# Performance work log

Hardware: AMD Instinct MI355X
Metric: run time of the kernel (lower is better)

## Reference

```python
import jax, jax.numpy as jnp
import numpy as np

N = 50000
E = 800000
IN_CH = 128
HIDDEN = 32
HEADS = 4
OUT_CH = 64
NEG_SLOPE = 0.2


def setup_inputs() -> dict:
    key = jax.random.key(0)
    ks = jax.random.split(key, 12)
    x = jax.random.normal(ks[0], (N, IN_CH), dtype=jnp.float32)
    edge_index = jax.random.randint(ks[1], (2, E), 0, N, dtype=jnp.int64)
    # layer 1: GATConv(IN_CH, HIDDEN, heads=4, concat=True)
    s1 = 1.0 / np.sqrt(IN_CH)
    W1 = jax.random.normal(ks[2], (IN_CH, HEADS * HIDDEN), dtype=jnp.float32) * s1
    att_src1 = jax.random.normal(ks[3], (HEADS, HIDDEN), dtype=jnp.float32) * 0.1
    att_dst1 = jax.random.normal(ks[4], (HEADS, HIDDEN), dtype=jnp.float32) * 0.1
    b1 = jnp.zeros((HEADS * HIDDEN,), dtype=jnp.float32)
    # layer 2: GATConv(HEADS*HIDDEN, OUT_CH, heads=1, concat=False)
    s2 = 1.0 / np.sqrt(HEADS * HIDDEN)
    W2 = jax.random.normal(ks[5], (HEADS * HIDDEN, OUT_CH), dtype=jnp.float32) * s2
    att_src2 = jax.random.normal(ks[6], (1, OUT_CH), dtype=jnp.float32) * 0.1
    att_dst2 = jax.random.normal(ks[7], (1, OUT_CH), dtype=jnp.float32) * 0.1
    b2 = jnp.zeros((OUT_CH,), dtype=jnp.float32)
    return {"x": x, "edge_index": edge_index, "W1": W1, "att_src1": att_src1,
            "att_dst1": att_dst1, "b1": b1, "W2": W2, "att_src2": att_src2,
            "att_dst2": att_dst2, "b2": b2}


def gat_conv(x, src, dst, W, a_src, a_dst, bias, heads, out_ch, concat):
    n = x.shape[0]
    h = (x @ W).reshape(n, heads, out_ch)               # [N, H, C]
    alpha_s = jnp.sum(h * a_src[None], axis=-1)          # [N, H]
    alpha_d = jnp.sum(h * a_dst[None], axis=-1)          # [N, H]
    e = alpha_s[src] + alpha_d[dst]                      # [E, H]
    e = jnp.where(e > 0, e, NEG_SLOPE * e)               # leaky_relu(0.2)
    # segment softmax over incoming edges of each dst node
    e_max = jax.ops.segment_max(e, dst, num_segments=n)
    e_max = jnp.where(jnp.isfinite(e_max), e_max, 0.0)
    ex = jnp.exp(e - e_max[dst])
    denom = jax.ops.segment_sum(ex, dst, num_segments=n)
    alpha = ex / (denom[dst] + 1e-16)                    # [E, H]
    msg = h[src] * alpha[:, :, None]                     # [E, H, C]
    out = jax.ops.segment_sum(msg, dst, num_segments=n)  # [N, H, C]
    if concat:
        out = out.reshape(n, heads * out_ch)
    else:
        out = out.mean(axis=1)
    return out + bias


def reference(x, edge_index, W1, att_src1, att_dst1, b1, W2, att_src2, att_dst2, b2):
    n = x.shape[0]
    loop = jnp.arange(n, dtype=edge_index.dtype)
    src = jnp.concatenate([edge_index[0], loop])  # add self-loops (PyG default)
    dst = jnp.concatenate([edge_index[1], loop])
    h = gat_conv(x, src, dst, W1, att_src1, att_dst1, b1, HEADS, HIDDEN, True)
    h = jax.nn.elu(h)
    return gat_conv(h, src, dst, W2, att_src2, att_dst2, b2, 1, OUT_CH, False)
```

## Files before the change

kernel.cpp:

```cpp
#include <hip/hip_runtime.h>

#define NN    50000
#define NE    800000
#define NET   850000
#define NBUCK ((NN + 255) / 256)
#define MAXB  8192
#define BINB  256
#define AGGB  3125

typedef __fp16 half2_t __attribute__((ext_vector_type(2)));
typedef _Float16 half8 __attribute__((ext_vector_type(8)));
typedef float floatx4 __attribute__((ext_vector_type(4)));

__device__ __forceinline__ float lrelu(float v) { return fmaxf(v, 0.2f * v); }
__device__ __forceinline__ unsigned pk16(float a, float b) {
    half2_t h = __builtin_amdgcn_cvt_pkrtz(a, b);
    return __builtin_bit_cast(unsigned, h);
}
__device__ __forceinline__ float2 unpk16(unsigned u) {
    half2_t h = __builtin_bit_cast(half2_t, u);
    return make_float2((float)h.x, (float)h.y);
}

__global__ __launch_bounds__(256) void gemm1_mfma_kernel(
    const float* __restrict__ x, const _Float16* __restrict__ w1t,
    const float* __restrict__ att_s, const float* __restrict__ att_d,
    _Float16* __restrict__ h1h, float* __restrict__ as, float* __restrict__ ad)
{
    __shared__ _Float16 lw[128 * 128];
    __shared__ _Float16 hs[64 * 128];
    const int t    = threadIdx.x;
    const int lane = t & 63;
    const int m    = lane & 15;
    const int q    = lane >> 4;
    const int wv   = t >> 6;
    const int gr0  = blockIdx.x * 64;
    const int rbase = gr0 + wv * 16;

    const int rme = rbase + m;
    const int rc  = rme < NN ? rme : NN - 1;
    const float* ap = x + (size_t)rc * 128 + q * 8;

    float4 f0[4], f1[4];
#pragma unroll
    for (int ks = 0; ks < 4; ks++) {
        f0[ks] = *(const float4*)(ap + ks * 32);
        f1[ks] = *(const float4*)(ap + ks * 32 + 4);
    }

    {
        const int kb = t & 15;
        const int n0 = t >> 4;
#pragma unroll
        for (int it = 0; it < 8; it++) {
            const int n = n0 + it * 16;
            const uint4 v = *(const uint4*)(w1t + n * 128 + kb * 8);
            *(uint4*)((char*)lw + n * 256 + ((kb * 16) ^ ((n & 7) << 4))) = v;
        }
    }
    __syncthreads();

    floatx4 acc[8];
#pragma unroll
    for (int nt = 0; nt < 8; nt++) acc[nt] = (floatx4){0.f, 0.f, 0.f, 0.f};

    const int swz = (m & 7) << 4;
#pragma unroll
    for (int ks = 0; ks < 4; ks++) {
        const uint4 au = make_uint4(pk16(f0[ks].x, f0[ks].y), pk16(f0[ks].z, f0[ks].w),
                                    pk16(f1[ks].x, f1[ks].y), pk16(f1[ks].z, f1[ks].w));
        const half8 a = __builtin_bit_cast(half8, au);
#pragma unroll
        for (int nt = 0; nt < 8; nt++) {
            const int n = nt * 16 + m;
            const half8 b = *(const half8*)((const char*)lw + n * 256 +
                                            ((ks * 64 + q * 16) ^ swz));
            acc[nt] = __builtin_amdgcn_mfma_f32_16x16x32_f16(a, b, acc[nt], 0, 0, 0);
        }
    }

    const int lrow0 = wv * 16 + q * 4;
#pragma unroll
    for (int nt = 0; nt < 8; nt++)
#pragma unroll
        for (int r = 0; r < 4; r++)
            hs[(lrow0 + r) * 128 + nt * 16 + m] = (_Float16)acc[nt][r];
    __syncthreads();

#pragma unroll
    for (int i = t; i < 1024; i += 256) {
        const int row = i >> 4;
        if (gr0 + row < NN)
            ((half8*)h1h)[(size_t)(gr0 + row) * 16 + (i & 15)] = ((const half8*)hs)[i];
    }

    const int arow = t >> 2, hd = t & 3;
    const int grow = gr0 + arow;
    float ps = 0.f, pd = 0.f;
    const half8*  hp8 = (const half8*)(hs + arow * 128 + hd * 32);
    const float4* s4  = (const float4*)(att_s + hd * 32);
    const float4* d4  = (const float4*)(att_d + hd * 32);
#pragma unroll
    for (int cc = 0; cc < 4; cc++) {
        const half8 hv = hp8[cc];
        const float4 a = s4[cc * 2], b = s4[cc * 2 + 1];
        const float4 c = d4[cc * 2], e = d4[cc * 2 + 1];
        ps += (float)hv[0]*a.x + (float)hv[1]*a.y + (float)hv[2]*a.z + (float)hv[3]*a.w
            + (float)hv[4]*b.x + (float)hv[5]*b.y + (float)hv[6]*b.z + (float)hv[7]*b.w;
        pd += (float)hv[0]*c.x + (float)hv[1]*c.y + (float)hv[2]*c.z + (float)hv[3]*c.w
            + (float)hv[4]*e.x + (float)hv[5]*e.y + (float)hv[6]*e.z + (float)hv[7]*e.w;
    }
    if (grow < NN) {
        as[grow * 4 + hd] = ps;
        ad[grow * 4 + hd] = pd;
    }
}

__global__ __launch_bounds__(256) void gemm2_mfma_kernel(
    const _Float16* __restrict__ ah, const _Float16* __restrict__ w2t,
    const float* __restrict__ att_s, const float* __restrict__ att_d,
    _Float16* __restrict__ h2h, float* __restrict__ as, float* __restrict__ ad)
{
    __shared__ _Float16 lw[64 * 128];
    __shared__ _Float16 hs[64 * 64];
    const int t    = threadIdx.x;
    const int lane = t & 63;
    const int m    = lane & 15;
    const int q    = lane >> 4;
    const int wv   = t >> 6;
    const int gr0  = blockIdx.x * 64;
    const int rbase = gr0 + wv * 16;

    const int rme = rbase + m;
    const int rc  = rme < NN ? rme : NN - 1;
    const _Float16* ap = ah + (size_t)rc * 128 + q * 8;

    half8 av[4];
#pragma unroll
    for (int ks = 0; ks < 4; ks++) av[ks] = *(const half8*)(ap + ks * 32);

    {
        const int kb = t & 15;
        const int n0 = t >> 4;
#pragma unroll
        for (int it = 0; it < 4; it++) {
            const int n = n0 + it * 16;
            const uint4 v = *(const uint4*)(w2t + n * 128 + kb * 8);
            *(uint4*)((char*)lw + n * 256 + ((kb * 16) ^ ((n & 7) << 4))) = v;
        }
    }
    __syncthreads();

    floatx4 acc[4];
#pragma unroll
    for (int nt = 0; nt < 4; nt++) acc[nt] = (floatx4){0.f, 0.f, 0.f, 0.f};

    const int swz = (m & 7) << 4;
#pragma unroll
    for (int ks = 0; ks < 4; ks++) {
#pragma unroll
        for (int nt = 0; nt < 4; nt++) {
            const int n = nt * 16 + m;
            const half8 b = *(const half8*)((const char*)lw + n * 256 +
                                            ((ks * 64 + q * 16) ^ swz));
            acc[nt] = __builtin_amdgcn_mfma_f32_16x16x32_f16(av[ks], b, acc[nt], 0, 0, 0);
        }
    }

    const int lrow0 = wv * 16 + q * 4;
#pragma unroll
    for (int nt = 0; nt < 4; nt++)
#pragma unroll
        for (int r = 0; r < 4; r++)
            hs[(lrow0 + r) * 64 + nt * 16 + m] = (_Float16)acc[nt][r];
    __syncthreads();

#pragma unroll
    for (int i = t; i < 512; i += 256) {
        const int row = i >> 3;
        if (gr0 + row < NN)
            ((half8*)h2h)[(size_t)(gr0 + row) * 8 + (i & 7)] = ((const half8*)hs)[i];
    }

    const int arow = t >> 2, sg = t & 3;
    const int grow = gr0 + arow;
    float ps = 0.f, pd = 0.f;
    const half8*  hp8 = (const half8*)(hs + arow * 64 + sg * 16);
    const float4* s4  = (const float4*)(att_s + sg * 16);
    const float4* d4  = (const float4*)(att_d + sg * 16);
#pragma unroll
    for (int cc = 0; cc < 2; cc++) {
        const half8 hv = hp8[cc];
        const float4 a = s4[cc * 2], b = s4[cc * 2 + 1];
        const float4 c = d4[cc * 2], e = d4[cc * 2 + 1];
        ps += (float)hv[0]*a.x + (float)hv[1]*a.y + (float)hv[2]*a.z + (float)hv[3]*a.w
            + (float)hv[4]*b.x + (float)hv[5]*b.y + (float)hv[6]*b.z + (float)hv[7]*b.w;
        pd += (float)hv[0]*c.x + (float)hv[1]*c.y + (float)hv[2]*c.z + (float)hv[3]*c.w
            + (float)hv[4]*e.x + (float)hv[5]*e.y + (float)hv[6]*e.z + (float)hv[7]*e.w;
    }
    ps += __shfl_down(ps, 2);  pd += __shfl_down(pd, 2);
    ps += __shfl_down(ps, 1);  pd += __shfl_down(pd, 1);
    if (sg == 0 && grow < NN) { as[grow] = ps; ad[grow] = pd; }
}

__global__ __launch_bounds__(1024) void bin_kernel(const int* __restrict__ ei,
                                                   const float* __restrict__ W1,
                                                   const float* __restrict__ W2,
                                                   _Float16* __restrict__ w1t,
                                                   _Float16* __restrict__ w2t,
                                                   int* __restrict__ bcnt,
                                                   unsigned* __restrict__ pairs)
{
    if (blockIdx.x < 24) {
        const int idx = blockIdx.x * 1024 + threadIdx.x;
        if (idx < 16384) {
            const int k = idx >> 7, n = idx & 127;
            w1t[n * 128 + k] = (_Float16)W1[idx];
        } else {
            const int j = idx - 16384;
            const int k = j >> 6, n = j & 63;
            w2t[n * 128 + k] = (_Float16)W2[j];
        }
    }

    __shared__ int hist[NBUCK], base[NBUCK], cur[NBUCK];
    const int t = threadIdx.x;
    if (t < NBUCK) { hist[t] = 0; cur[t] = 0; }
    __syncthreads();

    for (int e = blockIdx.x * 1024 + t; e < NET; e += BINB * 1024) {
        const int d = (e < NE) ? ei[NE + e] : (e - NE);
        atomicAdd(&hist[d >> 8], 1);
    }
    __syncthreads();
    if (t < NBUCK && hist[t]) base[t] = atomicAdd(&bcnt[t * 16], hist[t]);
    __syncthreads();
    for (int e = blockIdx.x * 1024 + t; e < NET; e += BINB * 1024) {
        int s, d;
        if (e < NE) { s = ei[e]; d = ei[NE + e]; } else { s = d = e - NE; }
        const int bk = d >> 8;
        const int r = atomicAdd(&cur[bk], 1);
        pairs[(size_t)bk * MAXB + base[bk] + r] =
            (unsigned)s | ((unsigned)(d & 255) << 16);
    }
}

__global__ __launch_bounds__(1024) void bsort_kernel(
    const int* __restrict__ bcnt, const unsigned* __restrict__ pairs,
    int* __restrict__ row_beg, int* __restrict__ row_end,
    int* __restrict__ col)
{
    __shared__ int hist[256], cur[256], sh[256];
    __shared__ int outl[MAXB];
    const int b = blockIdx.x, t = threadIdx.x;
    const int m = bcnt[b * 16];
    const int gbase = b * MAXB;
    if (t < 256) hist[t] = 0;
    __syncthreads();
    for (int i = t; i < m; i += 1024)
        atomicAdd(&hist[pairs[gbase + i] >> 16], 1);
    __syncthreads();
    if (t < 256) sh[t] = hist[t];
    __syncthreads();
#pragma unroll
    for (int off = 1; off < 256; off <<= 1) {
        int u = (t < 256 && t >= off) ? sh[t - off] : 0;
        __syncthreads();
        if (t < 256) sh[t] += u;
        __syncthreads();
    }
    if (t < 256) {
        const int ex = sh[t] - hist[t];
        cur[t] = ex;
        const int node = (b << 8) + t;
        if (node < NN) {
            row_beg[node] = gbase + ex;
            row_end[node] = gbase + ex + hist[t];
        }
    }
    __syncthreads();
    for (int i = t; i < m; i += 1024) {
        const unsigned p = pairs[gbase + i];
        const int r = atomicAdd(&cur[p >> 16], 1);
        outl[r] = (int)(p & 0xFFFFu);
    }
    __syncthreads();
    for (int i = t; i < m; i += 1024) col[gbase + i] = outl[i];
}

__global__ __launch_bounds__(1024) void agg1_fused_kernel(
    const int* __restrict__ row_beg, const int* __restrict__ row_end,
    const int* __restrict__ col, const unsigned* __restrict__ hh,
    const float* __restrict__ as1, const float* __restrict__ ad1,
    const float* __restrict__ b1, unsigned* __restrict__ acth)
{
    __shared__ float wbuf[16][64 * 4];
    const int wv   = threadIdx.x >> 6;
    const int d    = __builtin_amdgcn_readfirstlane(blockIdx.x * 16 + wv);
    const int lane = threadIdx.x & 63;
    const int head = lane >> 4;
    const int beg = row_beg[d], end = row_end[d];
    const float4 ad4 = ((const float4*)ad1)[d];
    float* wb = wbuf[wv];

    float acc0 = 0.f, acc1 = 0.f, den = 0.f;

    for (int jb = beg; jb < end; jb += 64) {
        const int cnt = min(64, end - jb);
        {
            const int sl = col[jb + min(lane, cnt - 1)];
            const float4 a = ((const float4*)as1)[sl];
            float4 w4;
            w4.x = __expf(lrelu(a.x + ad4.x));
            w4.y = __expf(lrelu(a.y + ad4.y));
            w4.z = __expf(lrelu(a.z + ad4.z));
            w4.w = __expf(lrelu(a.w + ad4.w));
            ((float4*)wb)[lane] = w4;
        }
        __asm__ volatile("s_waitcnt lgkmcnt(0)" ::: "memory");

        int k = 0;
        for (; k + 16 <= cnt; k += 16) {
            float    w[16];
            unsigned g[16];
#pragma unroll
            for (int u = 0; u < 16; u++) {
                const int s = col[jb + k + u];
                w[u] = wb[(k + u) * 4 + head];
                g[u] = hh[s * 64 + lane];
            }
#pragma unroll
            for (int u = 0; u < 16; u++) {
                const float2 g2 = unpk16(g[u]);
                den  += w[u];
                acc0 += w[u] * g2.x;
                acc1 += w[u] * g2.y;
            }
        }
        for (; k + 4 <= cnt; k += 4) {
            float    w[4];
            unsigned g[4];
#pragma unroll
            for (int u = 0; u < 4; u++) {
                const int s = col[jb + k + u];
                w[u] = wb[(k + u) * 4 + head];
                g[u] = hh[s * 64 + lane];
            }
#pragma unroll
            for (int u = 0; u < 4; u++) {
                const float2 g2 = unpk16(g[u]);
                den  += w[u];
                acc0 += w[u] * g2.x;
                acc1 += w[u] * g2.y;
            }
        }
        for (; k < cnt; k++) {
            const float w = wb[k * 4 + head];
            const float2 g2 = unpk16(hh[col[jb + k] * 64 + lane]);
            den  += w;
            acc0 += w * g2.x;
            acc1 += w * g2.y;
        }
        __asm__ volatile("" ::: "memory");
    }
    const float2 bb  = ((const float2*)b1)[lane];
    const float  inv = 1.f / (den + 1e-16f);
    float v0 = acc0 * inv + bb.x;
    float v1 = acc1 * inv + bb.y;
    v0 = v0 > 0.f ? v0 : (__expf(v0) - 1.f);
    v1 = v1 > 0.f ? v1 : (__expf(v1) - 1.f);
    acth[d * 64 + lane] = pk16(v0, v1);
}

__global__ __launch_bounds__(1024) void agg2_fused_kernel(
    const int* __restrict__ row_beg, const int* __restrict__ row_end,
    const int* __restrict__ col, const _Float16* __restrict__ h,
    const float* __restrict__ as2, const float* __restrict__ ad2,
    const float* __restrict__ b2, float* __restrict__ out)
{
    __shared__ float wbuf[16][64];
    const int wv   = threadIdx.x >> 6;
    const int d    = __builtin_amdgcn_readfirstlane(blockIdx.x * 16 + wv);
    const int lane = threadIdx.x & 63;
    const int half = lane >> 5;
    const int c    = lane & 31;
    const int beg = row_beg[d], end = row_end[d];
    const float add = ad2[d];
    float* wb = wbuf[wv];
    const unsigned* __restrict__ h2 = (const unsigned*)h;

    float acc0 = 0.f, acc1 = 0.f, den = 0.f;

    for (int jb = beg; jb < end; jb += 64) {
        const int cnt = min(64, end - jb);
        {
            const int sl = col[jb + min(lane, cnt - 1)];
            wb[lane] = __expf(lrelu(as2[sl] + add));
        }
        __asm__ volatile("s_waitcnt lgkmcnt(0)" ::: "memory");

        int k = 0;
        for (; k + 16 <= cnt; k += 16) {
            float    w[8];
            unsigned g[8];
#pragma unroll
            for (int u = 0; u < 8; u++) {
                const int e = jb + k + 2 * u + half;
                const int s = col[e];
                w[u] = wb[k + 2 * u + half];
                g[u] = h2[(size_t)s * 32 + c];
            }
#pragma unroll
            for (int u = 0; u < 8; u++) {
                const float2 g2 = unpk16(g[u]);
                den  += w[u];
                acc0 += w[u] * g2.x;
                acc1 += w[u] * g2.y;
            }
        }
        for (; k < cnt; k += 2) {
            const int  e   = k + half;
            const bool ok  = e < cnt;
            const int  s   = col[jb + (ok ? e : cnt - 1)];
            const float w  = ok ? wb[e] : 0.f;
            const float2 g2 = unpk16(h2[(size_t)s * 32 + c]);
            den  += w;
            acc0 += w * g2.x;
            acc1 += w * g2.y;
        }
        __asm__ volatile("" ::: "memory");
    }
    acc0 += __shfl_xor(acc0, 32);
    acc1 += __shfl_xor(acc1, 32);
    den  += __shfl_xor(den, 32);

    if (half == 0) {
        const float inv = 1.f / (den + 1e-16f);
        const float2 bb = ((const float2*)b2)[c];
        float2 o;
        o.x = acc0 * inv + bb.x;
        o.y = acc1 * inv + bb.y;
        ((float2*)out)[(size_t)d * 32 + c] = o;
    }
}

extern "C" void kernel_launch(void* const* d_in, const int* in_sizes, int n_in,
                              void* d_out, int out_size, void* d_ws, size_t ws_size,
                              hipStream_t stream)
{
    const float* x    = (const float*)d_in[0];
    const int*   ei   = (const int*)  d_in[1];
    const float* W1   = (const float*)d_in[2];
    const float* at_s1= (const float*)d_in[3];
    const float* at_d1= (const float*)d_in[4];
    const float* b1   = (const float*)d_in[5];
    const float* W2   = (const float*)d_in[6];
    const float* at_s2= (const float*)d_in[7];
    const float* at_d2= (const float*)d_in[8];
    const float* b2   = (const float*)d_in[9];
    float*       out  = (float*)d_out;

    const size_t NPAD = (size_t)NBUCK * MAXB;

    float* fw   = (float*)d_ws;
    float* as1  = fw;
    float* ad1  = as1  + NN * 4;
    float* as2  = ad1  + NN * 4;
    float* ad2  = as2  + NN;
    _Float16* h1h   = (_Float16*)(ad2 + NN);
    _Float16* act1h = h1h  + (size_t)NN * 128;
    _Float16* h2h   = act1h+ (size_t)NN * 128;
    _Float16* w1t   = h2h  + (size_t)NN * 64;
    _Float16* w2t   = w1t  + 16384;
    int*   row_beg = (int*)(w2t + 8192);
    int*   row_end = row_beg + NN;
    int*   col     = row_end + NN;
    int*   bcnt    = col + NPAD;
    unsigned* pairs = (unsigned*)(bcnt + 4096);

    hipMemsetAsync(bcnt, 0, 4096 * sizeof(int), stream);

    const int gemm_grid = (NN + 63) / 64;

    bin_kernel  <<<BINB, 1024, 0, stream>>>(ei, W1, W2, w1t, w2t, bcnt, pairs);
    bsort_kernel<<<NBUCK, 1024, 0, stream>>>(bcnt, pairs, row_beg, row_end, col);

    gemm1_mfma_kernel<<<gemm_grid, 256, 0, stream>>>(x, w1t, at_s1, at_d1, h1h, as1, ad1);
    agg1_fused_kernel<<<AGGB, 1024, 0, stream>>>(row_beg, row_end, col,
                        (const unsigned*)h1h, as1, ad1, b1, (unsigned*)act1h);

    gemm2_mfma_kernel<<<gemm_grid, 256, 0, stream>>>(act1h, w2t, at_s2, at_d2, h2h, as2, ad2);
    agg2_fused_kernel<<<AGGB, 1024, 0, stream>>>(row_beg, row_end, col,
                        h2h, as2, ad2, b2, out);
}
```

Measured before the change: 206.5 us.

## Merge bucket sort and first GEMM into one launch; shrink aggregation blocks

The CSR bucket sort and the layer-1 MFMA GEMM are independent, so they now share one launch: the first NBUCK blocks sort and the remaining 782 blocks each compute a 64-row GEMM tile. This removes a kernel boundary and lets the two phases run at the same time. The aggregation kernels also drop from 1024-thread blocks (16 waves) to 256-thread blocks (4 waves), with the grid enlarged to match. That may improve occupancy and tail behaviour, but the merged kernel sizes every block for the larger GEMM shared-memory footprint, and the sort now runs with only 256 threads per block.

```diff
diff --git a/kernel.cpp b/kernel.cpp
--- a/kernel.cpp
+++ b/kernel.cpp
@@ -6,7 +6,7 @@
 #define NBUCK ((NN + 255) / 256)
 #define MAXB  8192
 #define BINB  256
-#define AGGB  3125
+#define GTILE 782
 
 typedef __fp16 half2_t __attribute__((ext_vector_type(2)));
 typedef _Float16 half8 __attribute__((ext_vector_type(8)));
@@ -20,187 +20,6 @@
 __device__ __forceinline__ float2 unpk16(unsigned u) {
     half2_t h = __builtin_bit_cast(half2_t, u);
     return make_float2((float)h.x, (float)h.y);
-}
-
-__global__ __launch_bounds__(256) void gemm1_mfma_kernel(
-    const float* __restrict__ x, const _Float16* __restrict__ w1t,
-    const float* __restrict__ att_s, const float* __restrict__ att_d,
-    _Float16* __restrict__ h1h, float* __restrict__ as, float* __restrict__ ad)
-{
-    __shared__ _Float16 lw[128 * 128];
-    __shared__ _Float16 hs[64 * 128];
-    const int t    = threadIdx.x;
-    const int lane = t & 63;
-    const int m    = lane & 15;
-    const int q    = lane >> 4;
-    const int wv   = t >> 6;
-    const int gr0  = blockIdx.x * 64;
-    const int rbase = gr0 + wv * 16;
-
-    const int rme = rbase + m;
-    const int rc  = rme < NN ? rme : NN - 1;
-    const float* ap = x + (size_t)rc * 128 + q * 8;
-
-    float4 f0[4], f1[4];
-#pragma unroll
-    for (int ks = 0; ks < 4; ks++) {
-        f0[ks] = *(const float4*)(ap + ks * 32);
-        f1[ks] = *(const float4*)(ap + ks * 32 + 4);
-    }
-
-    {
-        const int kb = t & 15;
-        const int n0 = t >> 4;
-#pragma unroll
-        for (int it = 0; it < 8; it++) {
-            const int n = n0 + it * 16;
-            const uint4 v = *(const uint4*)(w1t + n * 128 + kb * 8);
-            *(uint4*)((char*)lw + n * 256 + ((kb * 16) ^ ((n & 7) << 4))) = v;
-        }
-    }
-    __syncthreads();
-
-    floatx4 acc[8];
-#pragma unroll
-    for (int nt = 0; nt < 8; nt++) acc[nt] = (floatx4){0.f, 0.f, 0.f, 0.f};
-
-    const int swz = (m & 7) << 4;
-#pragma unroll
-    for (int ks = 0; ks < 4; ks++) {
-        const uint4 au = make_uint4(pk16(f0[ks].x, f0[ks].y), pk16(f0[ks].z, f0[ks].w),
-                                    pk16(f1[ks].x, f1[ks].y), pk16(f1[ks].z, f1[ks].w));
-        const half8 a = __builtin_bit_cast(half8, au);
-#pragma unroll
-        for (int nt = 0; nt < 8; nt++) {
-            const int n = nt * 16 + m;
-            const half8 b = *(const half8*)((const char*)lw + n * 256 +
-                                            ((ks * 64 + q * 16) ^ swz));
-            acc[nt] = __builtin_amdgcn_mfma_f32_16x16x32_f16(a, b, acc[nt], 0, 0, 0);
-        }
-    }
-
-    const int lrow0 = wv * 16 + q * 4;
-#pragma unroll
-    for (int nt = 0; nt < 8; nt++)
-#pragma unroll
-        for (int r = 0; r < 4; r++)
-            hs[(lrow0 + r) * 128 + nt * 16 + m] = (_Float16)acc[nt][r];
-    __syncthreads();
-
-#pragma unroll
-    for (int i = t; i < 1024; i += 256) {
-        const int row = i >> 4;
-        if (gr0 + row < NN)
-            ((half8*)h1h)[(size_t)(gr0 + row) * 16 + (i & 15)] = ((const half8*)hs)[i];
-    }
-
-    const int arow = t >> 2, hd = t & 3;
-    const int grow = gr0 + arow;
-    float ps = 0.f, pd = 0.f;
-    const half8*  hp8 = (const half8*)(hs + arow * 128 + hd * 32);
-    const float4* s4  = (const float4*)(att_s + hd * 32);
-    const float4* d4  = (const float4*)(att_d + hd * 32);
-#pragma unroll
-    for (int cc = 0; cc < 4; cc++) {
-        const half8 hv = hp8[cc];
-        const float4 a = s4[cc * 2], b = s4[cc * 2 + 1];
-        const float4 c = d4[cc * 2], e = d4[cc * 2 + 1];
-        ps += (float)hv[0]*a.x + (float)hv[1]*a.y + (float)hv[2]*a.z + (float)hv[3]*a.w
-            + (float)hv[4]*b.x + (float)hv[5]*b.y + (float)hv[6]*b.z + (float)hv[7]*b.w;
-        pd += (float)hv[0]*c.x + (float)hv[1]*c.y + (float)hv[2]*c.z + (float)hv[3]*c.w
-            + (float)hv[4]*e.x + (float)hv[5]*e.y + (float)hv[6]*e.z + (float)hv[7]*e.w;
-    }
-    if (grow < NN) {
-        as[grow * 4 + hd] = ps;
-        ad[grow * 4 + hd] = pd;
-    }
-}
-
-__global__ __launch_bounds__(256) void gemm2_mfma_kernel(
-    const _Float16* __restrict__ ah, const _Float16* __restrict__ w2t,
-    const float* __restrict__ att_s, const float* __restrict__ att_d,
-    _Float16* __restrict__ h2h, float* __restrict__ as, float* __restrict__ ad)
-{
-    __shared__ _Float16 lw[64 * 128];
-    __shared__ _Float16 hs[64 * 64];
-    const int t    = threadIdx.x;
-    const int lane = t & 63;
-    const int m    = lane & 15;
-    const int q    = lane >> 4;
-    const int wv   = t >> 6;
-    const int gr0  = blockIdx.x * 64;
-    const int rbase = gr0 + wv * 16;
-
-    const int rme = rbase + m;
-    const int rc  = rme < NN ? rme : NN - 1;
-    const _Float16* ap = ah + (size_t)rc * 128 + q * 8;
-
-    half8 av[4];
-#pragma unroll
-    for (int ks = 0; ks < 4; ks++) av[ks] = *(const half8*)(ap + ks * 32);
-
-    {
-        const int kb = t & 15;
-        const int n0 = t >> 4;
-#pragma unroll
-        for (int it = 0; it < 4; it++) {
-            const int n = n0 + it * 16;
-            const uint4 v = *(const uint4*)(w2t + n * 128 + kb * 8);
-            *(uint4*)((char*)lw + n * 256 + ((kb * 16) ^ ((n & 7) << 4))) = v;
-        }
-    }
-    __syncthreads();
-
-    floatx4 acc[4];
-#pragma unroll
-    for (int nt = 0; nt < 4; nt++) acc[nt] = (floatx4){0.f, 0.f, 0.f, 0.f};
-
-    const int swz = (m & 7) << 4;
-#pragma unroll
-    for (int ks = 0; ks < 4; ks++) {
-#pragma unroll
-        for (int nt = 0; nt < 4; nt++) {
-            const int n = nt * 16 + m;
-            const half8 b = *(const half8*)((const char*)lw + n * 256 +
-                                            ((ks * 64 + q * 16) ^ swz));
-            acc[nt] = __builtin_amdgcn_mfma_f32_16x16x32_f16(av[ks], b, acc[nt], 0, 0, 0);
-        }
-    }
-
-    const int lrow0 = wv * 16 + q * 4;
-#pragma unroll
-    for (int nt = 0; nt < 4; nt++)
-#pragma unroll
-        for (int r = 0; r < 4; r++)
-            hs[(lrow0 + r) * 64 + nt * 16 + m] = (_Float16)acc[nt][r];
-    __syncthreads();
-
-#pragma unroll
-    for (int i = t; i < 512; i += 256) {
-        const int row = i >> 3;
-        if (gr0 + row < NN)
-            ((half8*)h2h)[(size_t)(gr0 + row) * 8 + (i & 7)] = ((const half8*)hs)[i];
-    }
-
-    const int arow = t >> 2, sg = t & 3;
-    const int grow = gr0 + arow;
-    float ps = 0.f, pd = 0.f;
-    const half8*  hp8 = (const half8*)(hs + arow * 64 + sg * 16);
-    const float4* s4  = (const float4*)(att_s + sg * 16);
-    const float4* d4  = (const float4*)(att_d + sg * 16);
-#pragma unroll
-    for (int cc = 0; cc < 2; cc++) {
-        const half8 hv = hp8[cc];
-        const float4 a = s4[cc * 2], b = s4[cc * 2 + 1];
-        const float4 c = d4[cc * 2], e = d4[cc * 2 + 1];
-        ps += (float)hv[0]*a.x + (float)hv[1]*a.y + (float)hv[2]*a.z + (float)hv[3]*a.w
-            + (float)hv[4]*b.x + (float)hv[5]*b.y + (float)hv[6]*b.z + (float)hv[7]*b.w;
-        pd += (float)hv[0]*c.x + (float)hv[1]*c.y + (float)hv[2]*c.z + (float)hv[3]*c.w
-            + (float)hv[4]*e.x + (float)hv[5]*e.y + (float)hv[6]*e.z + (float)hv[7]*e.w;
-    }
-    ps += __shfl_down(ps, 2);  pd += __shfl_down(pd, 2);
-    ps += __shfl_down(ps, 1);  pd += __shfl_down(pd, 1);
-    if (sg == 0 && grow < NN) { as[grow] = ps; ad[grow] = pd; }
 }
 
 __global__ __launch_bounds__(1024) void bin_kernel(const int* __restrict__ ei,
@@ -245,58 +64,239 @@
     }
 }
 
-__global__ __launch_bounds__(1024) void bsort_kernel(
+__global__ __launch_bounds__(256) void bsortgemm1_kernel(
     const int* __restrict__ bcnt, const unsigned* __restrict__ pairs,
-    int* __restrict__ row_beg, int* __restrict__ row_end,
-    int* __restrict__ col)
-{
-    __shared__ int hist[256], cur[256], sh[256];
-    __shared__ int outl[MAXB];
-    const int b = blockIdx.x, t = threadIdx.x;
-    const int m = bcnt[b * 16];
-    const int gbase = b * MAXB;
-    if (t < 256) hist[t] = 0;
+    int* __restrict__ row_beg, int* __restrict__ row_end, int* __restrict__ col,
+    const float* __restrict__ x, const _Float16* __restrict__ w1t,
+    const float* __restrict__ att_s, const float* __restrict__ att_d,
+    _Float16* __restrict__ h1h, float* __restrict__ as, float* __restrict__ ad)
+{
+    __shared__ __align__(16) char smem[49152];
+    const int t = threadIdx.x;
+
+    if (blockIdx.x < NBUCK) {
+        const int b = blockIdx.x;
+        int* hist = (int*)smem;
+        int* cur  = hist + 256;
+        int* sh   = cur + 256;
+        int* outl = sh + 256;
+        const int m = bcnt[b * 16];
+        const int gbase = b * MAXB;
+        hist[t] = 0;
+        __syncthreads();
+        for (int i = t; i < m; i += 256)
+            atomicAdd(&hist[pairs[gbase + i] >> 16], 1);
+        __syncthreads();
+        sh[t] = hist[t];
+        __syncthreads();
+#pragma unroll
+        for (int off = 1; off < 256; off <<= 1) {
+            const int u = (t >= off) ? sh[t - off] : 0;
+            __syncthreads();
+            sh[t] += u;
+            __syncthreads();
+        }
+        {
+            const int ex = sh[t] - hist[t];
+            cur[t] = ex;
+            const int node = (b << 8) + t;
+            if (node < NN) {
+                row_beg[node] = gbase + ex;
+                row_end[node] = gbase + ex + hist[t];
+            }
+        }
+        __syncthreads();
+        for (int i = t; i < m; i += 256) {
+            const unsigned p = pairs[gbase + i];
+            const int r = atomicAdd(&cur[p >> 16], 1);
+            outl[r] = (int)(p & 0xFFFFu);
+        }
+        __syncthreads();
+        for (int i = t; i < m; i += 256) col[gbase + i] = outl[i];
+    } else {
+        const int tile = blockIdx.x - NBUCK;
+        _Float16* lw = (_Float16*)smem;
+        _Float16* hs = (_Float16*)(smem + 32768);
+        const int lane = t & 63;
+        const int m    = lane & 15;
+        const int q    = lane >> 4;
+        const int wv   = t >> 6;
+        const int gr0  = tile * 64;
+        const int rme  = gr0 + wv * 16 + m;
+        const int rc   = rme < NN ? rme : NN - 1;
+        const float* ap = x + (size_t)rc * 128 + q * 8;
+
+        float4 f0[4], f1[4];
+#pragma unroll
+        for (int ks = 0; ks < 4; ks++) {
+            f0[ks] = *(const float4*)(ap + ks * 32);
+            f1[ks] = *(const float4*)(ap + ks * 32 + 4);
+        }
+        {
+            const int kb = t & 15;
+            const int n0 = t >> 4;
+#pragma unroll
+            for (int it = 0; it < 8; it++) {
+                const int n = n0 + it * 16;
+                const uint4 v = *(const uint4*)(w1t + n * 128 + kb * 8);
+                *(uint4*)((char*)lw + n * 256 + ((kb * 16) ^ ((n & 7) << 4))) = v;
+            }
+        }
+        __syncthreads();
+
+        floatx4 acc[8];
+#pragma unroll
+        for (int nt = 0; nt < 8; nt++) acc[nt] = (floatx4){0.f, 0.f, 0.f, 0.f};
+
+        const int swz = (m & 7) << 4;
+#pragma unroll
+        for (int ks = 0; ks < 4; ks++) {
+            const uint4 au = make_uint4(pk16(f0[ks].x, f0[ks].y), pk16(f0[ks].z, f0[ks].w),
+                                        pk16(f1[ks].x, f1[ks].y), pk16(f1[ks].z, f1[ks].w));
+            const half8 a = __builtin_bit_cast(half8, au);
+#pragma unroll
+            for (int nt = 0; nt < 8; nt++) {
+                const int n = nt * 16 + m;
+                const half8 b = *(const half8*)((const char*)lw + n * 256 +
+                                                ((ks * 64 + q * 16) ^ swz));
+                acc[nt] = __builtin_amdgcn_mfma_f32_16x16x32_f16(a, b, acc[nt], 0, 0, 0);
+            }
+        }
+
+        const int lrow0 = wv * 16 + q * 4;
+#pragma unroll
+        for (int nt = 0; nt < 8; nt++)
+#pragma unroll
+            for (int r = 0; r < 4; r++)
+                hs[(lrow0 + r) * 128 + nt * 16 + m] = (_Float16)acc[nt][r];
+        __syncthreads();
+
+#pragma unroll
+        for (int i = t; i < 1024; i += 256) {
+            const int row = i >> 4;
+            if (gr0 + row < NN)
+                ((half8*)h1h)[(size_t)(gr0 + row) * 16 + (i & 15)] = ((const half8*)hs)[i];
+        }
+
+        const int arow = t >> 2, hd = t & 3;
+        const int grow = gr0 + arow;
+        float ps = 0.f, pd = 0.f;
+        const half8*  hp8 = (const half8*)(hs + arow * 128 + hd * 32);
+        const float4* s4  = (const float4*)(att_s + hd * 32);
+        const float4* d4  = (const float4*)(att_d + hd * 32);
+#pragma unroll
+        for (int cc = 0; cc < 4; cc++) {
+            const half8 hv = hp8[cc];
+            const float4 a = s4[cc * 2], b = s4[cc * 2 + 1];
+            const float4 c = d4[cc * 2], e = d4[cc * 2 + 1];
+            ps += (float)hv[0]*a.x + (float)hv[1]*a.y + (float)hv[2]*a.z + (float)hv[3]*a.w
+                + (float)hv[4]*b.x + (float)hv[5]*b.y + (float)hv[6]*b.z + (float)hv[7]*b.w;
+            pd += (float)hv[0]*c.x + (float)hv[1]*c.y + (float)hv[2]*c.z + (float)hv[3]*c.w
+                + (float)hv[4]*e.x + (float)hv[5]*e.y + (float)hv[6]*e.z + (float)hv[7]*e.w;
+        }
+        if (grow < NN) {
+            as[grow * 4 + hd] = ps;
+            ad[grow * 4 + hd] = pd;
+        }
+    }
+}
+
+__global__ __launch_bounds__(256) void gemm2_mfma_kernel(
+    const _Float16* __restrict__ ah, const _Float16* __restrict__ w2t,
+    const float* __restrict__ att_s, const float* __restrict__ att_d,
+    _Float16* __restrict__ h2h, float* __restrict__ as, float* __restrict__ ad)
+{
+    __shared__ _Float16 lw[64 * 128];
+    __shared__ _Float16 hs[64 * 64];
+    const int t    = threadIdx.x;
+    const int lane = t & 63;
+    const int m    = lane & 15;
+    const int q    = lane >> 4;
+    const int wv   = t >> 6;
+    const int gr0  = blockIdx.x * 64;
+    const int rbase = gr0 + wv * 16;
+
+    const int rme = rbase + m;
+    const int rc  = rme < NN ? rme : NN - 1;
+    const _Float16* ap = ah + (size_t)rc * 128 + q * 8;
+
+    half8 av[4];
+#pragma unroll
+    for (int ks = 0; ks < 4; ks++) av[ks] = *(const half8*)(ap + ks * 32);
+
+    {
+        const int kb = t & 15;
+        const int n0 = t >> 4;
+#pragma unroll
+        for (int it = 0; it < 4; it++) {
+            const int n = n0 + it * 16;
+            const uint4 v = *(const uint4*)(w2t + n * 128 + kb * 8);
+            *(uint4*)((char*)lw + n * 256 + ((kb * 16) ^ ((n & 7) << 4))) = v;
+        }
+    }
     __syncthreads();
-    for (int i = t; i < m; i += 1024)
-        atomicAdd(&hist[pairs[gbase + i] >> 16], 1);
+
+    floatx4 acc[4];
+#pragma unroll
+    for (int nt = 0; nt < 4; nt++) acc[nt] = (floatx4){0.f, 0.f, 0.f, 0.f};
+
+    const int swz = (m & 7) << 4;
+#pragma unroll
+    for (int ks = 0; ks < 4; ks++) {
+#pragma unroll
+        for (int nt = 0; nt < 4; nt++) {
+            const int n = nt * 16 + m;
+            const half8 b = *(const half8*)((const char*)lw + n * 256 +
+                                            ((ks * 64 + q * 16) ^ swz));
+            acc[nt] = __builtin_amdgcn_mfma_f32_16x16x32_f16(av[ks], b, acc[nt], 0, 0, 0);
+        }
+    }
+
+    const int lrow0 = wv * 16 + q * 4;
+#pragma unroll
+    for (int nt = 0; nt < 4; nt++)
+#pragma unroll
+        for (int r = 0; r < 4; r++)
+            hs[(lrow0 + r) * 64 + nt * 16 + m] = (_Float16)acc[nt][r];
     __syncthreads();
-    if (t < 256) sh[t] = hist[t];
-    __syncthreads();
-#pragma unroll
-    for (int off = 1; off < 256; off <<= 1) {
-        int u = (t < 256 && t >= off) ? sh[t - off] : 0;
-        __syncthreads();
-        if (t < 256) sh[t] += u;
-        __syncthreads();
-    }
-    if (t < 256) {
-        const int ex = sh[t] - hist[t];
-        cur[t] = ex;
-        const int node = (b << 8) + t;
-        if (node < NN) {
-            row_beg[node] = gbase + ex;
-            row_end[node] = gbase + ex + hist[t];
-        }
-    }
-    __syncthreads();
-    for (int i = t; i < m; i += 1024) {
-        const unsigned p = pairs[gbase + i];
-        const int r = atomicAdd(&cur[p >> 16], 1);
-        outl[r] = (int)(p & 0xFFFFu);
-    }
-    __syncthreads();
-    for (int i = t; i < m; i += 1024) col[gbase + i] = outl[i];
-}
-
-__global__ __launch_bounds__(1024) void agg1_fused_kernel(
+
+#pragma unroll
+    for (int i = t; i < 512; i += 256) {
+        const int row = i >> 3;
+        if (gr0 + row < NN)
+            ((half8*)h2h)[(size_t)(gr0 + row) * 8 + (i & 7)] = ((const half8*)hs)[i];
+    }
+
+    const int arow = t >> 2, sg = t & 3;
+    const int grow = gr0 + arow;
+    float ps = 0.f, pd = 0.f;
+    const half8*  hp8 = (const half8*)(hs + arow * 64 + sg * 16);
+    const float4* s4  = (const float4*)(att_s + sg * 16);
+    const float4* d4  = (const float4*)(att_d + sg * 16);
+#pragma unroll
+    for (int cc = 0; cc < 2; cc++) {
+        const half8 hv = hp8[cc];
+        const float4 a = s4[cc * 2], b = s4[cc * 2 + 1];
+        const float4 c = d4[cc * 2], e = d4[cc * 2 + 1];
+        ps += (float)hv[0]*a.x + (float)hv[1]*a.y + (float)hv[2]*a.z + (float)hv[3]*a.w
+            + (float)hv[4]*b.x + (float)hv[5]*b.y + (float)hv[6]*b.z + (float)hv[7]*b.w;
+        pd += (float)hv[0]*c.x + (float)hv[1]*c.y + (float)hv[2]*c.z + (float)hv[3]*c.w
+            + (float)hv[4]*e.x + (float)hv[5]*e.y + (float)hv[6]*e.z + (float)hv[7]*e.w;
+    }
+    ps += __shfl_down(ps, 2);  pd += __shfl_down(pd, 2);
+    ps += __shfl_down(ps, 1);  pd += __shfl_down(pd, 1);
+    if (sg == 0 && grow < NN) { as[grow] = ps; ad[grow] = pd; }
+}
+
+__global__ __launch_bounds__(256) void agg1_fused_kernel(
     const int* __restrict__ row_beg, const int* __restrict__ row_end,
     const int* __restrict__ col, const unsigned* __restrict__ hh,
     const float* __restrict__ as1, const float* __restrict__ ad1,
     const float* __restrict__ b1, unsigned* __restrict__ acth)
 {
-    __shared__ float wbuf[16][64 * 4];
+    __shared__ float wbuf[4][64 * 4];
     const int wv   = threadIdx.x >> 6;
-    const int d    = __builtin_amdgcn_readfirstlane(blockIdx.x * 16 + wv);
+    const int d    = __builtin_amdgcn_readfirstlane((blockIdx.x * 256 + threadIdx.x) >> 6);
     const int lane = threadIdx.x & 63;
     const int head = lane >> 4;
     const int beg = row_beg[d], end = row_end[d];
@@ -372,15 +372,15 @@
     acth[d * 64 + lane] = pk16(v0, v1);
 }
 
-__global__ __launch_bounds__(1024) void agg2_fused_kernel(
+__global__ __launch_bounds__(256) void agg2_fused_kernel(
     const int* __restrict__ row_beg, const int* __restrict__ row_end,
     const int* __restrict__ col, const _Float16* __restrict__ h,
     const float* __restrict__ as2, const float* __restrict__ ad2,
     const float* __restrict__ b2, float* __restrict__ out)
 {
-    __shared__ float wbuf[16][64];
+    __shared__ float wbuf[4][64];
     const int wv   = threadIdx.x >> 6;
-    const int d    = __builtin_amdgcn_readfirstlane(blockIdx.x * 16 + wv);
+    const int d    = __builtin_amdgcn_readfirstlane(blockIdx.x * 4 + wv);
     const int lane = threadIdx.x & 63;
     const int half = lane >> 5;
     const int c    = lane & 31;
@@ -480,16 +480,18 @@
 
     hipMemsetAsync(bcnt, 0, 4096 * sizeof(int), stream);
 
-    const int gemm_grid = (NN + 63) / 64;
-
-    bin_kernel  <<<BINB, 1024, 0, stream>>>(ei, W1, W2, w1t, w2t, bcnt, pairs);
-    bsort_kernel<<<NBUCK, 1024, 0, stream>>>(bcnt, pairs, row_beg, row_end, col);
-
-    gemm1_mfma_kernel<<<gemm_grid, 256, 0, stream>>>(x, w1t, at_s1, at_d1, h1h, as1, ad1);
-    agg1_fused_kernel<<<AGGB, 1024, 0, stream>>>(row_beg, row_end, col,
+    const int node_wave_grid = NN / 4;
+
+    bin_kernel<<<BINB, 1024, 0, stream>>>(ei, W1, W2, w1t, w2t, bcnt, pairs);
+
+    bsortgemm1_kernel<<<NBUCK + GTILE, 256, 0, stream>>>(
+        bcnt, pairs, row_beg, row_end, col,
+        x, w1t, at_s1, at_d1, h1h, as1, ad1);
+
+    agg1_fused_kernel<<<node_wave_grid, 256, 0, stream>>>(row_beg, row_end, col,
                         (const unsigned*)h1h, as1, ad1, b1, (unsigned*)act1h);
 
-    gemm2_mfma_kernel<<<gemm_grid, 256, 0, stream>>>(act1h, w2t, at_s2, at_d2, h2h, as2, ad2);
-    agg2_fused_kernel<<<AGGB, 1024, 0, stream>>>(row_beg, row_end, col,
+    gemm2_mfma_kernel<<<(NN + 63) / 64, 256, 0, stream>>>(act1h, w2t, at_s2, at_d2, h2h, as2, ad2);
+    agg2_fused_kernel<<<node_wave_grid, 256, 0, stream>>>(row_beg, row_end, col,
                         h2h, as2, ad2, b2, out);
 }
```

New measurement: 195.7 us. 1.05x faster.
